# Optimization experiments

Measured on AMD Instinct MI355X. Metric: run time of the kernel, lower is better.

The kernel has to match this reference:

```python
import jax, jax.numpy as jnp
import numpy as np

EPS = 1e-5

def setup_inputs() -> dict:
    key = jax.random.key(0)
    ks = jax.random.split(key, 4)
    B, C, H, W = 16, 256, 64, 64
    x = jax.random.normal(ks[0], (B, C, H, W), dtype=jnp.float32)
    w_qkv = jax.random.normal(ks[1], (3 * C, C), dtype=jnp.float32) * (C ** -0.5)
    w_proj = jax.random.normal(ks[2], (C, C), dtype=jnp.float32) * (C ** -0.5)
    b_proj = jnp.zeros((C,), dtype=jnp.float32)
    gamma = jnp.ones((C,), dtype=jnp.float32)
    beta = jnp.zeros((C,), dtype=jnp.float32)
    return {"x": x, "w_qkv": w_qkv, "w_proj": w_proj, "b_proj": b_proj,
            "gamma": gamma, "beta": beta}

def reference(x, w_qkv, w_proj, b_proj, gamma, beta):
    B, C, H, W = x.shape
    num_heads = 8
    head_dim = C // num_heads
    scale = head_dim ** -0.5
    # LayerNorm over channels (applied in BHWC layout)
    xc = x.transpose(0, 2, 3, 1)                       # (B,H,W,C)
    mu = xc.mean(axis=-1, keepdims=True)
    var = ((xc - mu) ** 2).mean(axis=-1, keepdims=True)
    xn = (xc - mu) * jax.lax.rsqrt(var + EPS) * gamma + beta
    # 1x1 conv qkv: (B,H,W,C) x (3C,C) -> (B,H,W,3C)
    qkv = jnp.einsum('bhwc,dc->bhwd', xn, w_qkv)
    qkv = qkv.reshape(B, H, W, 3, num_heads, head_dim)
    q, k, v = qkv[..., 0, :, :], qkv[..., 1, :, :], qkv[..., 2, :, :]  # (B,H,W,nh,hd)
    # attention along the W axis, independently per (batch, head, row H)
    attn = jnp.einsum('bhqnd,bhknd->bhnqk', q, k) * scale   # (B,H,nh,W,W)
    attn = jax.nn.softmax(attn, axis=-1)
    out = jnp.einsum('bhnqk,bhknd->bhqnd', attn, v)          # (B,H,W,nh,hd)
    out = out.reshape(B, H, W, C)
    # 1x1 conv proj
    out = jnp.einsum('bhwc,dc->bhwd', out, w_proj) + b_proj
    return out.transpose(0, 3, 1, 2)                         # (B,C,H,W)
```

## Files before the change

### kernel.cpp

```cpp
#include <hip/hip_runtime.h>

typedef _Float16 f16;
typedef _Float16 f16x8 __attribute__((ext_vector_type(8)));
typedef float f32x4 __attribute__((ext_vector_type(4)));

#define XNS 264
#define QKS 40
#define VTS 72
#define PSS 72

__device__ __forceinline__ f32x4 mfma16(f16x8 a, f16x8 b, f32x4 c){
  return __builtin_amdgcn_mfma_f32_16x16x32_f16(a, b, c, 0, 0, 0);
}

__global__ __launch_bounds__(256) void k_cvt(const float* __restrict__ wqkv,
                                             const float* __restrict__ wproj,
                                             f16* __restrict__ wqkv_h,
                                             f16* __restrict__ wproj_h){
  int i = blockIdx.x*256 + threadIdx.x;
  for (int idx = i; idx < 768*256; idx += gridDim.x*256) wqkv_h[idx] = (f16)wqkv[idx];
  for (int idx = i; idx < 256*256; idx += gridDim.x*256) wproj_h[idx] = (f16)wproj[idx];
}

__global__ __launch_bounds__(512) void k_fused(const float* __restrict__ x,
    const float* __restrict__ gamma, const float* __restrict__ beta,
    const f16* __restrict__ wqkv, const f16* __restrict__ wproj,
    const float* __restrict__ bproj, float* __restrict__ out)
{
  __shared__ f16 xn[64*XNS];
  __shared__ f16 perw[8][7424];
  __shared__ float red[2][8][64];
  __shared__ float mrs[2][64];

  const int t = threadIdx.x;
  const int lane = t & 63;
  const int h = t >> 6;
  const int l15 = lane & 15, l16 = lane >> 4;
  const int row = blockIdx.x;
  const int b = row >> 6, hh = row & 63;
  const float* xrow = x + (size_t)b*256*4096 + hh*64;

  {
    float s = 0.f, s2 = 0.f;
    for (int i = 0; i < 32; ++i){
      float v = xrow[(size_t)(h*32 + i)*4096 + lane];
      s += v; s2 += v*v;
    }
    red[0][h][lane] = s; red[1][h][lane] = s2;
  }
  __syncthreads();
  if (t < 64){
    float ss = 0.f, qq = 0.f;
    for (int j = 0; j < 8; ++j){ ss += red[0][j][t]; qq += red[1][j][t]; }
    float mu = ss*(1.f/256.f);
    float var = qq*(1.f/256.f) - mu*mu;
    mrs[0][t] = mu; mrs[1][t] = rsqrtf(var + 1e-5f);
  }
  __syncthreads();

  {
    float mu = mrs[0][lane], rs = mrs[1][lane];
    for (int i = 0; i < 32; ++i){
      int c = h*32 + i;
      float v = xrow[(size_t)c*4096 + lane];
      xn[lane*XNS + c] = (f16)((v - mu)*rs*gamma[c] + beta[c]);
    }
  }
  __syncthreads();

  f16* qs  = &perw[h][0];
  f16* ks  = &perw[h][2560];
  f16* vts = &perw[h][5120];

  for (int qk = 0; qk < 2; ++qk){
    const f16* wb = wqkv + (size_t)(qk*256 + h*32)*256;
    f32x4 acc[4][2] = {};
    for (int kk = 0; kk < 8; ++kk){
      int k0 = kk*32 + l16*8;
      f16x8 a[4], bb[2];
      for (int m = 0; m < 4; ++m) a[m]  = *(const f16x8*)&xn[(m*16 + l15)*XNS + k0];
      for (int n = 0; n < 2; ++n) bb[n] = *(const f16x8*)&wb[(size_t)(n*16 + l15)*256 + k0];
      for (int m = 0; m < 4; ++m)
        for (int n = 0; n < 2; ++n)
          acc[m][n] = mfma16(a[m], bb[n], acc[m][n]);
    }
    f16* dst = qk ? ks : qs;
    for (int m = 0; m < 4; ++m)
      for (int n = 0; n < 2; ++n)
        for (int r = 0; r < 4; ++r){
          int pos = m*16 + l16*4 + r;
          int d   = n*16 + l15;
          dst[pos*QKS + d] = (f16)acc[m][n][r];
        }
  }
  {
    const f16* wv = wqkv + (size_t)(512 + h*32)*256;
    f32x4 acc[2][4] = {};
    for (int kk = 0; kk < 8; ++kk){
      int k0 = kk*32 + l16*8;
      f16x8 a[2], bb[4];
      for (int m = 0; m < 2; ++m) a[m]  = *(const f16x8*)&wv[(size_t)(m*16 + l15)*256 + k0];
      for (int n = 0; n < 4; ++n) bb[n] = *(const f16x8*)&xn[(n*16 + l15)*XNS + k0];
      for (int m = 0; m < 2; ++m)
        for (int n = 0; n < 4; ++n)
          acc[m][n] = mfma16(a[m], bb[n], acc[m][n]);
    }
    for (int m = 0; m < 2; ++m)
      for (int n = 0; n < 4; ++n)
        for (int r = 0; r < 4; ++r){
          int d   = m*16 + l16*4 + r;
          int pos = n*16 + l15;
          vts[d*VTS + pos] = (f16)acc[m][n][r];
        }
  }
  __syncthreads();

  f32x4 sa[4][4];
  {
    int k0 = l16*8;
    f16x8 a[4], bb[4];
    for (int m = 0; m < 4; ++m) a[m]  = *(const f16x8*)&qs[(m*16 + l15)*QKS + k0];
    for (int n = 0; n < 4; ++n) bb[n] = *(const f16x8*)&ks[(n*16 + l15)*QKS + k0];
    f32x4 z = {0.f,0.f,0.f,0.f};
    for (int m = 0; m < 4; ++m)
      for (int n = 0; n < 4; ++n)
        sa[m][n] = mfma16(a[m], bb[n], z);
  }
  f16* ps = &perw[h][0];
  {
    const float sc = 0.17677669529663687f;
    for (int m = 0; m < 4; ++m)
      for (int r = 0; r < 4; ++r){
        float mx = fmaxf(fmaxf(sa[m][0][r], sa[m][1][r]), fmaxf(sa[m][2][r], sa[m][3][r]));
        mx = fmaxf(mx, __shfl_xor(mx, 1));
        mx = fmaxf(mx, __shfl_xor(mx, 2));
        mx = fmaxf(mx, __shfl_xor(mx, 4));
        mx = fmaxf(mx, __shfl_xor(mx, 8));
        float pv[4]; float sum = 0.f;
        for (int n = 0; n < 4; ++n){ float p = __expf((sa[m][n][r] - mx)*sc); pv[n] = p; sum += p; }
        sum += __shfl_xor(sum, 1);
        sum += __shfl_xor(sum, 2);
        sum += __shfl_xor(sum, 4);
        sum += __shfl_xor(sum, 8);
        float inv = 1.f/sum;
        int q = m*16 + l16*4 + r;
        for (int n = 0; n < 4; ++n) ps[q*PSS + n*16 + l15] = (f16)(pv[n]*inv);
      }
  }
  __syncthreads();

  f16* al = xn;
  {
    f32x4 oa[4][2] = {};
    for (int kk = 0; kk < 2; ++kk){
      int k0 = kk*32 + l16*8;
      f16x8 a[4], bb[2];
      for (int m = 0; m < 4; ++m) a[m]  = *(const f16x8*)&ps[(m*16 + l15)*PSS + k0];
      for (int n = 0; n < 2; ++n) bb[n] = *(const f16x8*)&vts[(n*16 + l15)*VTS + k0];
      for (int m = 0; m < 4; ++m)
        for (int n = 0; n < 2; ++n)
          oa[m][n] = mfma16(a[m], bb[n], oa[m][n]);
    }
    for (int m = 0; m < 4; ++m)
      for (int n = 0; n < 2; ++n)
        for (int r = 0; r < 4; ++r){
          int pos = m*16 + l16*4 + r;
          al[pos*XNS + h*32 + n*16 + l15] = (f16)oa[m][n][r];
        }
  }
  __syncthreads();

  {
    f32x4 acc[4][2] = {};
    for (int kk = 0; kk < 8; ++kk){
      int k0 = kk*32 + l16*8;
      f16x8 a[4], bb[2];
      for (int m = 0; m < 4; ++m) a[m]  = *(const f16x8*)&al[(m*16 + l15)*XNS + k0];
      for (int n = 0; n < 2; ++n) bb[n] = *(const f16x8*)&wproj[(size_t)(h*32 + n*16 + l15)*256 + k0];
      for (int m = 0; m < 4; ++m)
        for (int n = 0; n < 2; ++n)
          acc[m][n] = mfma16(a[m], bb[n], acc[m][n]);
    }
    float bia[2];
    for (int n = 0; n < 2; ++n) bia[n] = bproj[h*32 + n*16 + l15];
    __syncthreads();
    float* ol = (float*)&perw[h][0];
    for (int n = 0; n < 2; ++n)
      for (int m = 0; m < 4; ++m)
        for (int r = 0; r < 4; ++r)
          ol[(n*16 + l15)*65 + m*16 + l16*4 + r] = acc[m][n][r] + bia[n];
    __syncthreads();
    float* orow = out + ((size_t)b*256 + h*32)*4096 + hh*64;
    for (int rr = 0; rr < 32; ++rr)
      orow[(size_t)rr*4096 + lane] = ol[rr*65 + lane];
  }
}

extern "C" void kernel_launch(void* const* d_in, const int* in_sizes, int n_in,
                              void* d_out, int out_size, void* d_ws, size_t ws_size,
                              hipStream_t stream)
{
  const float* x     = (const float*)d_in[0];
  const float* wqkv  = (const float*)d_in[1];
  const float* wproj = (const float*)d_in[2];
  const float* bproj = (const float*)d_in[3];
  const float* gamma = (const float*)d_in[4];
  const float* beta  = (const float*)d_in[5];
  float* out = (float*)d_out;

  f16* ws = (f16*)d_ws;
  f16* wqkv_h  = ws;
  f16* wproj_h = ws + 196608;

  k_cvt  <<<256, 256, 0, stream>>>(wqkv, wproj, wqkv_h, wproj_h);
  k_fused<<<1024, 512, 0, stream>>>(x, gamma, beta, wqkv_h, wproj_h, bproj, out);
}
```

Measured before the change: 216.9 us.

## Process heads in pairs across waves to shrink LDS and raise occupancy

Shared memory use drops because only two heads' Q/K/V/P buffers are held at once instead of eight. The eight waves now split each head pair four ways over query rows, and the projection GEMM is accumulated incrementally across head-pair iterations. x is read once with float4 loads into LDS and normalized in place instead of being read twice from global memory. Output is written directly with 16-byte stores, skipping the LDS transpose. Costs are more barriers per block, four serial iterations, and LayerNorm statistics computed from f16-rounded values, which may reduce accuracy.

Result: slower. 283.8 us (+30.8%).

```diff
diff --git a/kernel.cpp b/kernel.cpp
--- a/kernel.cpp
+++ b/kernel.cpp
@@ -8,6 +8,7 @@
 #define QKS 40
 #define VTS 72
 #define PSS 72
+#define ALS 72
 
 __device__ __forceinline__ f32x4 mfma16(f16x8 a, f16x8 b, f32x4 c){
   return __builtin_amdgcn_mfma_f32_16x16x32_f16(a, b, c, 0, 0, 0);
@@ -22,177 +23,191 @@
   for (int idx = i; idx < 256*256; idx += gridDim.x*256) wproj_h[idx] = (f16)wproj[idx];
 }
 
-__global__ __launch_bounds__(512) void k_fused(const float* __restrict__ x,
+__global__ __launch_bounds__(512, 4) void k_fused(const float* __restrict__ x,
     const float* __restrict__ gamma, const float* __restrict__ beta,
     const f16* __restrict__ wqkv, const f16* __restrict__ wproj,
     const float* __restrict__ bproj, float* __restrict__ out)
 {
-  __shared__ f16 xn[64*XNS];
-  __shared__ f16 perw[8][7424];
-  __shared__ float red[2][8][64];
-  __shared__ float mrs[2][64];
+  __shared__ __align__(16) f16 xn[64*XNS];
+  __shared__ __align__(16) f16 slot[2][7424];
+  __shared__ __align__(16) f16 alit[64*ALS];
+  float* red = (float*)&slot[0][0];
+  float* mrs = (float*)&slot[0][2048];
 
   const int t = threadIdx.x;
   const int lane = t & 63;
   const int h = t >> 6;
+  const int s = h >> 2, ws = h & 3;
   const int l15 = lane & 15, l16 = lane >> 4;
   const int row = blockIdx.x;
   const int b = row >> 6, hh = row & 63;
   const float* xrow = x + (size_t)b*256*4096 + hh*64;
 
   {
-    float s = 0.f, s2 = 0.f;
-    for (int i = 0; i < 32; ++i){
-      float v = xrow[(size_t)(h*32 + i)*4096 + lane];
-      s += v; s2 += v*v;
-    }
-    red[0][h][lane] = s; red[1][h][lane] = s2;
+    int c = t >> 1, wh = t & 1;
+    const float4* src = (const float4*)(xrow + (size_t)c*4096 + wh*32);
+    for (int j = 0; j < 8; ++j){
+      float4 v = src[j];
+      int w = wh*32 + j*4;
+      xn[(w+0)*XNS + c] = (f16)v.x;
+      xn[(w+1)*XNS + c] = (f16)v.y;
+      xn[(w+2)*XNS + c] = (f16)v.z;
+      xn[(w+3)*XNS + c] = (f16)v.w;
+    }
+  }
+  __syncthreads();
+
+  {
+    float ssum = 0.f, s2 = 0.f;
+    for (int j8 = 0; j8 < 4; ++j8){
+      f16x8 v = *(const f16x8*)&xn[lane*XNS + h*32 + j8*8];
+      for (int e = 0; e < 8; ++e){ float f = (float)v[e]; ssum += f; s2 += f*f; }
+    }
+    red[(0*8 + h)*64 + lane] = ssum;
+    red[(1*8 + h)*64 + lane] = s2;
   }
   __syncthreads();
   if (t < 64){
     float ss = 0.f, qq = 0.f;
-    for (int j = 0; j < 8; ++j){ ss += red[0][j][t]; qq += red[1][j][t]; }
+    for (int j = 0; j < 8; ++j){ ss += red[j*64 + t]; qq += red[(8+j)*64 + t]; }
     float mu = ss*(1.f/256.f);
     float var = qq*(1.f/256.f) - mu*mu;
-    mrs[0][t] = mu; mrs[1][t] = rsqrtf(var + 1e-5f);
-  }
-  __syncthreads();
-
-  {
-    float mu = mrs[0][lane], rs = mrs[1][lane];
-    for (int i = 0; i < 32; ++i){
-      int c = h*32 + i;
-      float v = xrow[(size_t)c*4096 + lane];
-      xn[lane*XNS + c] = (f16)((v - mu)*rs*gamma[c] + beta[c]);
-    }
-  }
-  __syncthreads();
-
-  f16* qs  = &perw[h][0];
-  f16* ks  = &perw[h][2560];
-  f16* vts = &perw[h][5120];
-
-  for (int qk = 0; qk < 2; ++qk){
-    const f16* wb = wqkv + (size_t)(qk*256 + h*32)*256;
-    f32x4 acc[4][2] = {};
-    for (int kk = 0; kk < 8; ++kk){
-      int k0 = kk*32 + l16*8;
-      f16x8 a[4], bb[2];
-      for (int m = 0; m < 4; ++m) a[m]  = *(const f16x8*)&xn[(m*16 + l15)*XNS + k0];
-      for (int n = 0; n < 2; ++n) bb[n] = *(const f16x8*)&wb[(size_t)(n*16 + l15)*256 + k0];
-      for (int m = 0; m < 4; ++m)
-        for (int n = 0; n < 2; ++n)
-          acc[m][n] = mfma16(a[m], bb[n], acc[m][n]);
-    }
-    f16* dst = qk ? ks : qs;
-    for (int m = 0; m < 4; ++m)
+    mrs[t] = mu; mrs[64 + t] = rsqrtf(var + 1e-5f);
+  }
+  __syncthreads();
+  {
+    float mu = mrs[lane], rs = mrs[64 + lane];
+    for (int j8 = 0; j8 < 4; ++j8){
+      f16x8 v = *(const f16x8*)&xn[lane*XNS + h*32 + j8*8];
+      f16x8 o;
+      for (int e = 0; e < 8; ++e){
+        int c = h*32 + j8*8 + e;
+        o[e] = (f16)(((float)v[e] - mu)*rs*gamma[c] + beta[c]);
+      }
+      *(f16x8*)&xn[lane*XNS + h*32 + j8*8] = o;
+    }
+  }
+  __syncthreads();
+
+  f16* qs  = &slot[s][0];
+  f16* ks  = &slot[s][2560];
+  f16* vts = &slot[s][5120];
+  f16* ps  = &slot[s][0];
+
+  f32x4 pacc[4][2] = {};
+
+  for (int iter = 0; iter < 4; ++iter){
+    const int head = iter*2 + s;
+    for (int qk = 0; qk < 2; ++qk){
+      const f16* wb = wqkv + (size_t)(qk*256 + head*32)*256;
+      f32x4 acc[2] = {};
+      for (int kk = 0; kk < 8; ++kk){
+        int k0 = kk*32 + l16*8;
+        f16x8 a  = *(const f16x8*)&xn[(ws*16 + l15)*XNS + k0];
+        f16x8 b0 = *(const f16x8*)&wb[(size_t)(l15)*256 + k0];
+        f16x8 b1 = *(const f16x8*)&wb[(size_t)(16 + l15)*256 + k0];
+        acc[0] = mfma16(a, b0, acc[0]);
+        acc[1] = mfma16(a, b1, acc[1]);
+      }
+      f16* dst = qk ? ks : qs;
       for (int n = 0; n < 2; ++n)
         for (int r = 0; r < 4; ++r){
-          int pos = m*16 + l16*4 + r;
-          int d   = n*16 + l15;
-          dst[pos*QKS + d] = (f16)acc[m][n][r];
-        }
-  }
-  {
-    const f16* wv = wqkv + (size_t)(512 + h*32)*256;
-    f32x4 acc[2][4] = {};
-    for (int kk = 0; kk < 8; ++kk){
-      int k0 = kk*32 + l16*8;
-      f16x8 a[2], bb[4];
-      for (int m = 0; m < 2; ++m) a[m]  = *(const f16x8*)&wv[(size_t)(m*16 + l15)*256 + k0];
-      for (int n = 0; n < 4; ++n) bb[n] = *(const f16x8*)&xn[(n*16 + l15)*XNS + k0];
-      for (int m = 0; m < 2; ++m)
-        for (int n = 0; n < 4; ++n)
-          acc[m][n] = mfma16(a[m], bb[n], acc[m][n]);
-    }
-    for (int m = 0; m < 2; ++m)
-      for (int n = 0; n < 4; ++n)
+          int pos = ws*16 + l16*4 + r;
+          dst[pos*QKS + n*16 + l15] = (f16)acc[n][r];
+        }
+    }
+    {
+      const f16* wv = wqkv + (size_t)(512 + head*32)*256;
+      int mV = ws >> 1, nB = (ws & 1)*2;
+      f32x4 acc[2] = {};
+      for (int kk = 0; kk < 8; ++kk){
+        int k0 = kk*32 + l16*8;
+        f16x8 a  = *(const f16x8*)&wv[(size_t)(mV*16 + l15)*256 + k0];
+        f16x8 b0 = *(const f16x8*)&xn[((nB+0)*16 + l15)*XNS + k0];
+        f16x8 b1 = *(const f16x8*)&xn[((nB+1)*16 + l15)*XNS + k0];
+        acc[0] = mfma16(a, b0, acc[0]);
+        acc[1] = mfma16(a, b1, acc[1]);
+      }
+      for (int n = 0; n < 2; ++n)
         for (int r = 0; r < 4; ++r){
-          int d   = m*16 + l16*4 + r;
-          int pos = n*16 + l15;
-          vts[d*VTS + pos] = (f16)acc[m][n][r];
-        }
-  }
-  __syncthreads();
-
-  f32x4 sa[4][4];
-  {
-    int k0 = l16*8;
-    f16x8 a[4], bb[4];
-    for (int m = 0; m < 4; ++m) a[m]  = *(const f16x8*)&qs[(m*16 + l15)*QKS + k0];
-    for (int n = 0; n < 4; ++n) bb[n] = *(const f16x8*)&ks[(n*16 + l15)*QKS + k0];
-    f32x4 z = {0.f,0.f,0.f,0.f};
-    for (int m = 0; m < 4; ++m)
-      for (int n = 0; n < 4; ++n)
-        sa[m][n] = mfma16(a[m], bb[n], z);
-  }
-  f16* ps = &perw[h][0];
-  {
-    const float sc = 0.17677669529663687f;
-    for (int m = 0; m < 4; ++m)
+          int d   = mV*16 + l16*4 + r;
+          int pos = (nB+n)*16 + l15;
+          vts[d*VTS + pos] = (f16)acc[n][r];
+        }
+    }
+    __syncthreads();
+
+    f32x4 sa[4];
+    {
+      f16x8 a = *(const f16x8*)&qs[(ws*16 + l15)*QKS + l16*8];
+      f32x4 z = {0.f,0.f,0.f,0.f};
+      for (int n = 0; n < 4; ++n){
+        f16x8 bb = *(const f16x8*)&ks[(n*16 + l15)*QKS + l16*8];
+        sa[n] = mfma16(a, bb, z);
+      }
+    }
+    __syncthreads();
+
+    {
+      const float sc = 0.17677669529663687f;
       for (int r = 0; r < 4; ++r){
-        float mx = fmaxf(fmaxf(sa[m][0][r], sa[m][1][r]), fmaxf(sa[m][2][r], sa[m][3][r]));
+        float mx = fmaxf(fmaxf(sa[0][r], sa[1][r]), fmaxf(sa[2][r], sa[3][r]));
         mx = fmaxf(mx, __shfl_xor(mx, 1));
         mx = fmaxf(mx, __shfl_xor(mx, 2));
         mx = fmaxf(mx, __shfl_xor(mx, 4));
         mx = fmaxf(mx, __shfl_xor(mx, 8));
-        float pv[4]; float sum = 0.f;
-        for (int n = 0; n < 4; ++n){ float p = __expf((sa[m][n][r] - mx)*sc); pv[n] = p; sum += p; }
+        float pv[4], sum = 0.f;
+        for (int n = 0; n < 4; ++n){ float p = __expf((sa[n][r] - mx)*sc); pv[n] = p; sum += p; }
         sum += __shfl_xor(sum, 1);
         sum += __shfl_xor(sum, 2);
         sum += __shfl_xor(sum, 4);
         sum += __shfl_xor(sum, 8);
         float inv = 1.f/sum;
-        int q = m*16 + l16*4 + r;
+        int q = ws*16 + l16*4 + r;
         for (int n = 0; n < 4; ++n) ps[q*PSS + n*16 + l15] = (f16)(pv[n]*inv);
       }
-  }
-  __syncthreads();
-
-  f16* al = xn;
-  {
-    f32x4 oa[4][2] = {};
+    }
+    {
+      f32x4 oa[2] = {};
+      for (int kk = 0; kk < 2; ++kk){
+        int k0 = kk*32 + l16*8;
+        f16x8 a = *(const f16x8*)&ps[(ws*16 + l15)*PSS + k0];
+        for (int n = 0; n < 2; ++n){
+          f16x8 bb = *(const f16x8*)&vts[(n*16 + l15)*VTS + k0];
+          oa[n] = mfma16(a, bb, oa[n]);
+        }
+      }
+      for (int n = 0; n < 2; ++n)
+        for (int r = 0; r < 4; ++r){
+          int pos = ws*16 + l16*4 + r;
+          alit[pos*ALS + s*32 + n*16 + l15] = (f16)oa[n][r];
+        }
+    }
+    __syncthreads();
+
     for (int kk = 0; kk < 2; ++kk){
       int k0 = kk*32 + l16*8;
       f16x8 a[4], bb[2];
-      for (int m = 0; m < 4; ++m) a[m]  = *(const f16x8*)&ps[(m*16 + l15)*PSS + k0];
-      for (int n = 0; n < 2; ++n) bb[n] = *(const f16x8*)&vts[(n*16 + l15)*VTS + k0];
+      for (int m = 0; m < 4; ++m) a[m] = *(const f16x8*)&alit[(m*16 + l15)*ALS + k0];
+      for (int n = 0; n < 2; ++n)
+        bb[n] = *(const f16x8*)&wproj[(size_t)(h*32 + n*16 + l15)*256 + iter*64 + k0];
       for (int m = 0; m < 4; ++m)
         for (int n = 0; n < 2; ++n)
-          oa[m][n] = mfma16(a[m], bb[n], oa[m][n]);
-    }
-    for (int m = 0; m < 4; ++m)
-      for (int n = 0; n < 2; ++n)
-        for (int r = 0; r < 4; ++r){
-          int pos = m*16 + l16*4 + r;
-          al[pos*XNS + h*32 + n*16 + l15] = (f16)oa[m][n][r];
-        }
-  }
-  __syncthreads();
-
-  {
-    f32x4 acc[4][2] = {};
-    for (int kk = 0; kk < 8; ++kk){
-      int k0 = kk*32 + l16*8;
-      f16x8 a[4], bb[2];
-      for (int m = 0; m < 4; ++m) a[m]  = *(const f16x8*)&al[(m*16 + l15)*XNS + k0];
-      for (int n = 0; n < 2; ++n) bb[n] = *(const f16x8*)&wproj[(size_t)(h*32 + n*16 + l15)*256 + k0];
-      for (int m = 0; m < 4; ++m)
-        for (int n = 0; n < 2; ++n)
-          acc[m][n] = mfma16(a[m], bb[n], acc[m][n]);
-    }
+          pacc[m][n] = mfma16(a[m], bb[n], pacc[m][n]);
+    }
+  }
+
+  {
     float bia[2];
     for (int n = 0; n < 2; ++n) bia[n] = bproj[h*32 + n*16 + l15];
-    __syncthreads();
-    float* ol = (float*)&perw[h][0];
-    for (int n = 0; n < 2; ++n)
-      for (int m = 0; m < 4; ++m)
-        for (int r = 0; r < 4; ++r)
-          ol[(n*16 + l15)*65 + m*16 + l16*4 + r] = acc[m][n][r] + bia[n];
-    __syncthreads();
-    float* orow = out + ((size_t)b*256 + h*32)*4096 + hh*64;
-    for (int rr = 0; rr < 32; ++rr)
-      orow[(size_t)rr*4096 + lane] = ol[rr*65 + lane];
+    float* obase = out + (size_t)b*256*4096 + hh*64;
+    for (int m = 0; m < 4; ++m)
+      for (int n = 0; n < 2; ++n){
+        int dout = h*32 + n*16 + l15;
+        f32x4 v;
+        for (int r = 0; r < 4; ++r) v[r] = pacc[m][n][r] + bia[n];
+        *(f32x4*)&obase[(size_t)dout*4096 + m*16 + l16*4] = v;
+      }
   }
 }
 
```

## Stage x once in LDS, prefetch weights to registers, store output directly

Applied to the files above, without the earlier changes.

The input row is read from global memory once with float4 loads and staged as f16 in LDS. LayerNorm statistics and normalization are then computed from that copy instead of reading x twice. Q/K/V/proj weight fragments are preloaded into registers ahead of each GEMM, one barrier between softmax and PV is removed, and the output transpose through LDS is replaced by direct vectorized float4 stores. The launch bound asks for 2 blocks per CU, and loops are fully unrolled. In exchange, statistics are now computed from f16-rounded inputs, and the large register arrays risk spills or lower occupancy.

Result: faster. 211.4 us (-2.5%).

```diff
diff --git a/kernel.cpp b/kernel.cpp
--- a/kernel.cpp
+++ b/kernel.cpp
@@ -22,15 +22,15 @@
   for (int idx = i; idx < 256*256; idx += gridDim.x*256) wproj_h[idx] = (f16)wproj[idx];
 }
 
-__global__ __launch_bounds__(512) void k_fused(const float* __restrict__ x,
+__global__ __launch_bounds__(512, 2) void k_fused(const float* __restrict__ x,
     const float* __restrict__ gamma, const float* __restrict__ beta,
     const f16* __restrict__ wqkv, const f16* __restrict__ wproj,
     const float* __restrict__ bproj, float* __restrict__ out)
 {
-  __shared__ f16 xn[64*XNS];
-  __shared__ f16 perw[8][7424];
+  __shared__ __align__(16) f16 xn[64*XNS];
+  __shared__ __align__(16) f16 perw[8][7424];
   __shared__ float red[2][8][64];
-  __shared__ float mrs[2][64];
+  __shared__ float mrs2[2][64];
 
   const int t = threadIdx.x;
   const int lane = t & 63;
@@ -40,13 +40,44 @@
   const int b = row >> 6, hh = row & 63;
   const float* xrow = x + (size_t)b*256*4096 + hh*64;
 
-  {
-    float s = 0.f, s2 = 0.f;
-    for (int i = 0; i < 32; ++i){
-      float v = xrow[(size_t)(h*32 + i)*4096 + lane];
-      s += v; s2 += v*v;
-    }
-    red[0][h][lane] = s; red[1][h][lane] = s2;
+  f16x8 bq[16];
+  {
+    const f16* wq = wqkv + (size_t)(h*32)*256;
+    #pragma unroll
+    for (int n = 0; n < 2; ++n)
+      #pragma unroll
+      for (int kk = 0; kk < 8; ++kk)
+        bq[n*8+kk] = *(const f16x8*)&wq[(size_t)(n*16 + l15)*256 + kk*32 + l16*8];
+  }
+
+  {
+    float4 xv[8];
+    #pragma unroll
+    for (int it = 0; it < 8; ++it){
+      int c = it*32 + h*4 + l16;
+      xv[it] = *(const float4*)&xrow[(size_t)c*4096 + l15*4];
+    }
+    #pragma unroll
+    for (int it = 0; it < 8; ++it){
+      int c = it*32 + h*4 + l16;
+      int w0 = l15*4;
+      xn[(w0+0)*XNS + c] = (f16)xv[it].x;
+      xn[(w0+1)*XNS + c] = (f16)xv[it].y;
+      xn[(w0+2)*XNS + c] = (f16)xv[it].z;
+      xn[(w0+3)*XNS + c] = (f16)xv[it].w;
+    }
+  }
+  __syncthreads();
+
+  {
+    float ssum = 0.f, s2 = 0.f;
+    #pragma unroll
+    for (int j8 = 0; j8 < 4; ++j8){
+      f16x8 v = *(const f16x8*)&xn[lane*XNS + h*32 + j8*8];
+      #pragma unroll
+      for (int e = 0; e < 8; ++e){ float f = (float)v[e]; ssum += f; s2 += f*f; }
+    }
+    red[0][h][lane] = ssum; red[1][h][lane] = s2;
   }
   __syncthreads();
   if (t < 64){
@@ -54,16 +85,21 @@
     for (int j = 0; j < 8; ++j){ ss += red[0][j][t]; qq += red[1][j][t]; }
     float mu = ss*(1.f/256.f);
     float var = qq*(1.f/256.f) - mu*mu;
-    mrs[0][t] = mu; mrs[1][t] = rsqrtf(var + 1e-5f);
-  }
-  __syncthreads();
-
-  {
-    float mu = mrs[0][lane], rs = mrs[1][lane];
-    for (int i = 0; i < 32; ++i){
-      int c = h*32 + i;
-      float v = xrow[(size_t)c*4096 + lane];
-      xn[lane*XNS + c] = (f16)((v - mu)*rs*gamma[c] + beta[c]);
+    mrs2[0][t] = mu; mrs2[1][t] = rsqrtf(var + 1e-5f);
+  }
+  __syncthreads();
+  {
+    float mu = mrs2[0][lane], rs = mrs2[1][lane];
+    #pragma unroll
+    for (int j8 = 0; j8 < 4; ++j8){
+      f16x8 v = *(const f16x8*)&xn[lane*XNS + h*32 + j8*8];
+      f16x8 o;
+      #pragma unroll
+      for (int e = 0; e < 8; ++e){
+        int c = h*32 + j8*8 + e;
+        o[e] = (f16)(((float)v[e] - mu)*rs*gamma[c] + beta[c]);
+      }
+      *(f16x8*)&xn[lane*XNS + h*32 + j8*8] = o;
     }
   }
   __syncthreads();
@@ -71,40 +107,83 @@
   f16* qs  = &perw[h][0];
   f16* ks  = &perw[h][2560];
   f16* vts = &perw[h][5120];
-
-  for (int qk = 0; qk < 2; ++qk){
-    const f16* wb = wqkv + (size_t)(qk*256 + h*32)*256;
+  f16* ps  = &perw[h][0];
+
+  f16x8 bk[16];
+  {
+    const f16* wk = wqkv + (size_t)(256 + h*32)*256;
+    #pragma unroll
+    for (int n = 0; n < 2; ++n)
+      #pragma unroll
+      for (int kk = 0; kk < 8; ++kk)
+        bk[n*8+kk] = *(const f16x8*)&wk[(size_t)(n*16 + l15)*256 + kk*32 + l16*8];
+  }
+  {
     f32x4 acc[4][2] = {};
+    #pragma unroll
     for (int kk = 0; kk < 8; ++kk){
       int k0 = kk*32 + l16*8;
-      f16x8 a[4], bb[2];
-      for (int m = 0; m < 4; ++m) a[m]  = *(const f16x8*)&xn[(m*16 + l15)*XNS + k0];
-      for (int n = 0; n < 2; ++n) bb[n] = *(const f16x8*)&wb[(size_t)(n*16 + l15)*256 + k0];
+      f16x8 a[4];
+      #pragma unroll
+      for (int m = 0; m < 4; ++m) a[m] = *(const f16x8*)&xn[(m*16 + l15)*XNS + k0];
+      #pragma unroll
       for (int m = 0; m < 4; ++m)
+        #pragma unroll
         for (int n = 0; n < 2; ++n)
-          acc[m][n] = mfma16(a[m], bb[n], acc[m][n]);
-    }
-    f16* dst = qk ? ks : qs;
+          acc[m][n] = mfma16(a[m], bq[n*8+kk], acc[m][n]);
+    }
+    #pragma unroll
     for (int m = 0; m < 4; ++m)
       for (int n = 0; n < 2; ++n)
-        for (int r = 0; r < 4; ++r){
-          int pos = m*16 + l16*4 + r;
-          int d   = n*16 + l15;
-          dst[pos*QKS + d] = (f16)acc[m][n][r];
-        }
-  }
+        for (int r = 0; r < 4; ++r)
+          qs[(m*16 + l16*4 + r)*QKS + n*16 + l15] = (f16)acc[m][n][r];
+  }
+
+  f16x8 bv[16];
   {
     const f16* wv = wqkv + (size_t)(512 + h*32)*256;
+    #pragma unroll
+    for (int n = 0; n < 2; ++n)
+      #pragma unroll
+      for (int kk = 0; kk < 8; ++kk)
+        bv[n*8+kk] = *(const f16x8*)&wv[(size_t)(n*16 + l15)*256 + kk*32 + l16*8];
+  }
+  {
+    f32x4 acc[4][2] = {};
+    #pragma unroll
+    for (int kk = 0; kk < 8; ++kk){
+      int k0 = kk*32 + l16*8;
+      f16x8 a[4];
+      #pragma unroll
+      for (int m = 0; m < 4; ++m) a[m] = *(const f16x8*)&xn[(m*16 + l15)*XNS + k0];
+      #pragma unroll
+      for (int m = 0; m < 4; ++m)
+        #pragma unroll
+        for (int n = 0; n < 2; ++n)
+          acc[m][n] = mfma16(a[m], bk[n*8+kk], acc[m][n]);
+    }
+    #pragma unroll
+    for (int m = 0; m < 4; ++m)
+      for (int n = 0; n < 2; ++n)
+        for (int r = 0; r < 4; ++r)
+          ks[(m*16 + l16*4 + r)*QKS + n*16 + l15] = (f16)acc[m][n][r];
+  }
+
+  {
     f32x4 acc[2][4] = {};
+    #pragma unroll
     for (int kk = 0; kk < 8; ++kk){
       int k0 = kk*32 + l16*8;
-      f16x8 a[2], bb[4];
-      for (int m = 0; m < 2; ++m) a[m]  = *(const f16x8*)&wv[(size_t)(m*16 + l15)*256 + k0];
+      f16x8 bb[4];
+      #pragma unroll
       for (int n = 0; n < 4; ++n) bb[n] = *(const f16x8*)&xn[(n*16 + l15)*XNS + k0];
+      #pragma unroll
       for (int m = 0; m < 2; ++m)
+        #pragma unroll
         for (int n = 0; n < 4; ++n)
-          acc[m][n] = mfma16(a[m], bb[n], acc[m][n]);
-    }
+          acc[m][n] = mfma16(bv[m*8+kk], bb[n], acc[m][n]);
+    }
+    #pragma unroll
     for (int m = 0; m < 2; ++m)
       for (int n = 0; n < 4; ++n)
         for (int r = 0; r < 4; ++r){
@@ -113,30 +192,46 @@
           vts[d*VTS + pos] = (f16)acc[m][n][r];
         }
   }
+
+  f16x8 bp[16];
+  {
+    const f16* wp = wproj + (size_t)(h*32)*256;
+    #pragma unroll
+    for (int n = 0; n < 2; ++n)
+      #pragma unroll
+      for (int kk = 0; kk < 8; ++kk)
+        bp[n*8+kk] = *(const f16x8*)&wp[(size_t)(n*16 + l15)*256 + kk*32 + l16*8];
+  }
   __syncthreads();
 
   f32x4 sa[4][4];
   {
     int k0 = l16*8;
     f16x8 a[4], bb[4];
+    #pragma unroll
     for (int m = 0; m < 4; ++m) a[m]  = *(const f16x8*)&qs[(m*16 + l15)*QKS + k0];
+    #pragma unroll
     for (int n = 0; n < 4; ++n) bb[n] = *(const f16x8*)&ks[(n*16 + l15)*QKS + k0];
     f32x4 z = {0.f,0.f,0.f,0.f};
-    for (int m = 0; m < 4; ++m)
+    #pragma unroll
+    for (int m = 0; m < 4; ++m)
+      #pragma unroll
       for (int n = 0; n < 4; ++n)
         sa[m][n] = mfma16(a[m], bb[n], z);
   }
-  f16* ps = &perw[h][0];
   {
     const float sc = 0.17677669529663687f;
-    for (int m = 0; m < 4; ++m)
+    #pragma unroll
+    for (int m = 0; m < 4; ++m)
+      #pragma unroll
       for (int r = 0; r < 4; ++r){
         float mx = fmaxf(fmaxf(sa[m][0][r], sa[m][1][r]), fmaxf(sa[m][2][r], sa[m][3][r]));
         mx = fmaxf(mx, __shfl_xor(mx, 1));
         mx = fmaxf(mx, __shfl_xor(mx, 2));
         mx = fmaxf(mx, __shfl_xor(mx, 4));
         mx = fmaxf(mx, __shfl_xor(mx, 8));
-        float pv[4]; float sum = 0.f;
+        float pv[4], sum = 0.f;
+        #pragma unroll
         for (int n = 0; n < 4; ++n){ float p = __expf((sa[m][n][r] - mx)*sc); pv[n] = p; sum += p; }
         sum += __shfl_xor(sum, 1);
         sum += __shfl_xor(sum, 2);
@@ -144,23 +239,28 @@
         sum += __shfl_xor(sum, 8);
         float inv = 1.f/sum;
         int q = m*16 + l16*4 + r;
+        #pragma unroll
         for (int n = 0; n < 4; ++n) ps[q*PSS + n*16 + l15] = (f16)(pv[n]*inv);
       }
   }
-  __syncthreads();
-
   f16* al = xn;
   {
     f32x4 oa[4][2] = {};
+    #pragma unroll
     for (int kk = 0; kk < 2; ++kk){
       int k0 = kk*32 + l16*8;
       f16x8 a[4], bb[2];
+      #pragma unroll
       for (int m = 0; m < 4; ++m) a[m]  = *(const f16x8*)&ps[(m*16 + l15)*PSS + k0];
+      #pragma unroll
       for (int n = 0; n < 2; ++n) bb[n] = *(const f16x8*)&vts[(n*16 + l15)*VTS + k0];
+      #pragma unroll
       for (int m = 0; m < 4; ++m)
+        #pragma unroll
         for (int n = 0; n < 2; ++n)
           oa[m][n] = mfma16(a[m], bb[n], oa[m][n]);
     }
+    #pragma unroll
     for (int m = 0; m < 4; ++m)
       for (int n = 0; n < 2; ++n)
         for (int r = 0; r < 4; ++r){
@@ -172,27 +272,32 @@
 
   {
     f32x4 acc[4][2] = {};
+    #pragma unroll
     for (int kk = 0; kk < 8; ++kk){
       int k0 = kk*32 + l16*8;
-      f16x8 a[4], bb[2];
-      for (int m = 0; m < 4; ++m) a[m]  = *(const f16x8*)&al[(m*16 + l15)*XNS + k0];
-      for (int n = 0; n < 2; ++n) bb[n] = *(const f16x8*)&wproj[(size_t)(h*32 + n*16 + l15)*256 + k0];
+      f16x8 a[4];
+      #pragma unroll
+      for (int m = 0; m < 4; ++m) a[m] = *(const f16x8*)&al[(m*16 + l15)*XNS + k0];
+      #pragma unroll
       for (int m = 0; m < 4; ++m)
+        #pragma unroll
         for (int n = 0; n < 2; ++n)
-          acc[m][n] = mfma16(a[m], bb[n], acc[m][n]);
+          acc[m][n] = mfma16(a[m], bp[n*8+kk], acc[m][n]);
     }
     float bia[2];
+    #pragma unroll
     for (int n = 0; n < 2; ++n) bia[n] = bproj[h*32 + n*16 + l15];
-    __syncthreads();
-    float* ol = (float*)&perw[h][0];
-    for (int n = 0; n < 2; ++n)
-      for (int m = 0; m < 4; ++m)
-        for (int r = 0; r < 4; ++r)
-          ol[(n*16 + l15)*65 + m*16 + l16*4 + r] = acc[m][n][r] + bia[n];
-    __syncthreads();
-    float* orow = out + ((size_t)b*256 + h*32)*4096 + hh*64;
-    for (int rr = 0; rr < 32; ++rr)
-      orow[(size_t)rr*4096 + lane] = ol[rr*65 + lane];
+    float* obase = out + (size_t)b*256*4096 + hh*64;
+    #pragma unroll
+    for (int m = 0; m < 4; ++m)
+      #pragma unroll
+      for (int n = 0; n < 2; ++n){
+        int dout = h*32 + n*16 + l15;
+        f32x4 v;
+        #pragma unroll
+        for (int r = 0; r < 4; ++r) v[r] = acc[m][n][r] + bia[n];
+        *(f32x4*)&obase[(size_t)dout*4096 + m*16 + l16*4] = v;
+      }
   }
 }
 
```
